# Kernel tuning notes

Hardware: AMD Instinct MI355X
Metric: run time of the kernel (lower is better)

The kernel has to match this reference:

```python
import jax, jax.numpy as jnp
import numpy as np


def _soft_attention(h, context, W_in, W_out):
    """Luong soft-dot attention. h: [B,H], context: [B,L,H].
    W_in: [H,H] (in,out layout), W_out: [2H,H]."""
    target = h @ W_in                                  # [B, H]
    attn = jnp.einsum('blh,bh->bl', context, target)   # [B, L]
    p = jax.nn.softmax(attn, axis=-1)                  # [B, L]
    weighted_ctx = jnp.einsum('bl,blh->bh', p, context)  # [B, H]
    h_tilde = jnp.tanh(jnp.concatenate([weighted_ctx, h], axis=1) @ W_out)  # [B, H]
    return h_tilde, p


def setup_inputs() -> dict:
    key = jax.random.key(0)
    ks = jax.random.split(key, 13)
    B, L, H = 64, 512, 1024
    s2 = 1.0 / np.sqrt(2 * H)
    s1 = 1.0 / np.sqrt(H)
    return {
        'h_tilde_s': jax.random.normal(ks[0], (B, H), jnp.float32),
        'h_tilde_o': jax.random.normal(ks[1], (B, H), jnp.float32),
        'h_tilde_a': jax.random.normal(ks[2], (B, H), jnp.float32),
        'enc_out': jax.random.normal(ks[3], (B, L, H), jnp.float32),
        'full_feature_len': 36,
        'W_as': jax.random.normal(ks[4], (2 * H, H), jnp.float32) * s2,
        'W_so': jax.random.normal(ks[5], (2 * H, H), jnp.float32) * s2,
        'W_oa': jax.random.normal(ks[6], (2 * H, H), jnp.float32) * s2,
        'Win_as': jax.random.normal(ks[7], (H, H), jnp.float32) * s1,
        'Win_so': jax.random.normal(ks[8], (H, H), jnp.float32) * s1,
        'Win_oa': jax.random.normal(ks[9], (H, H), jnp.float32) * s1,
        'Wout_as': jax.random.normal(ks[10], (2 * H, H), jnp.float32) * s2,
        'Wout_so': jax.random.normal(ks[11], (2 * H, H), jnp.float32) * s2,
        'Wout_oa': jax.random.normal(ks[12], (2 * H, H), jnp.float32) * s2,
    }


def reference(h_tilde_s, h_tilde_o, h_tilde_a, enc_out, full_feature_len,
              W_as, W_so, W_oa, Win_as, Win_so, Win_oa,
              Wout_as, Wout_so, Wout_oa):
    # Relational contexts via concat + linear(no bias) + tanh
    h_as = jnp.tanh(jnp.concatenate([h_tilde_a, h_tilde_s], axis=1) @ W_as)  # [B,H]
    h_so = jnp.tanh(jnp.concatenate([h_tilde_s, h_tilde_o], axis=1) @ W_so)
    h_oa = jnp.tanh(jnp.concatenate([h_tilde_o, h_tilde_a], axis=1) @ W_oa)
    # Three parallel soft-dot attentions over encoder output
    sa_as, _ = _soft_attention(h_as, enc_out, Win_as, Wout_as)
    sa_so, _ = _soft_attention(h_so, enc_out, Win_so, Wout_so)
    sa_oa, _ = _soft_attention(h_oa, enc_out, Win_oa, Wout_oa)
    B, H = sa_as.shape
    F = full_feature_len
    # repeat_interleave of size-1 dim == broadcast tile to [B, F, H]
    ctx_mas = jnp.broadcast_to(sa_as[:, None, :], (B, F, H))
    ctx_mso = jnp.broadcast_to(sa_so[:, None, :], (B, F, H))
    ctx_moa = jnp.broadcast_to(sa_oa[:, None, :], (B, F, H))
    return (ctx_mas, ctx_mso, ctx_moa)
```

## Files before the change

### kernel.cpp

```cpp
#include <hip/hip_runtime.h>

constexpr int BB = 64;
constexpr int LL = 512;
constexpr int HH = 1024;
constexpr int SPLITS = 16;
constexpr int NTHR  = 256;
constexpr int NWORK_GEMM = 3 * 16 * SPLITS;

typedef float nt_float4 __attribute__((ext_vector_type(4)));

struct Args {
    const float* hs; const float* ho; const float* ha; const float* enc;
    const int* Fp;
    const float* W_as;  const float* W_so;  const float* W_oa;
    const float* Win_as; const float* Win_so; const float* Win_oa;
    const float* Wout_as; const float* Wout_so; const float* Wout_oa;
    float* partA; float* partC; float* partG;
    float* hx; float* wc; float* opm; float* ms;
    float* out;
};

template<int K0, int K1>
__device__ __forceinline__ void gemm_tile(const float* __restrict__ a0,
                                          const float* __restrict__ a1,
                                          const float* __restrict__ w,
                                          float* __restrict__ part_r,
                                          int nt, int sp, int tid,
                                          float (*As)[64], float (*Ws)[64])
{
    constexpr int K = K0 + K1;
    constexpr int KRANGE = K / SPLITS;
    const int n0 = nt << 6;
    const int ks = sp * KRANGE;
    const int tn = tid & 15;
    const int tm = tid >> 4;
    const int m   = tid >> 2;
    const int kk0 = (tid & 3) << 3;
    const int j4  = (tid & 15) << 2;
    const int kkw = tid >> 4;

    float4 av0, av1, wv0, wv1;
    {
        const int kg = ks + kk0;
        const float* srcA = (K1 == 0 || kg < K0) ? (a0 + (size_t)m * HH + kg)
                                                 : (a1 + (size_t)m * HH + (kg - K0));
        av0 = *(const float4*)srcA;
        av1 = *(const float4*)(srcA + 4);
        wv0 = *(const float4*)(w + (size_t)(ks + kkw) * HH + n0 + j4);
        wv1 = *(const float4*)(w + (size_t)(ks + kkw + 16) * HH + n0 + j4);
    }

    float acc[4][4] = {};

    for (int kt = ks; kt < ks + KRANGE; kt += 32) {
        As[kk0 + 0][m] = av0.x; As[kk0 + 1][m] = av0.y;
        As[kk0 + 2][m] = av0.z; As[kk0 + 3][m] = av0.w;
        As[kk0 + 4][m] = av1.x; As[kk0 + 5][m] = av1.y;
        As[kk0 + 6][m] = av1.z; As[kk0 + 7][m] = av1.w;
        *(float4*)&Ws[kkw][j4]      = wv0;
        *(float4*)&Ws[kkw + 16][j4] = wv1;
        __syncthreads();

        if (kt + 32 < ks + KRANGE) {
            const int kn = kt + 32;
            const int kg = kn + kk0;
            const float* srcA = (K1 == 0 || kg < K0) ? (a0 + (size_t)m * HH + kg)
                                                     : (a1 + (size_t)m * HH + (kg - K0));
            av0 = *(const float4*)srcA;
            av1 = *(const float4*)(srcA + 4);
            wv0 = *(const float4*)(w + (size_t)(kn + kkw) * HH + n0 + j4);
            wv1 = *(const float4*)(w + (size_t)(kn + kkw + 16) * HH + n0 + j4);
        }

        #pragma unroll
        for (int kk = 0; kk < 32; kk++) {
            float4 a4 = *(const float4*)&As[kk][tm << 2];
            float4 b4 = *(const float4*)&Ws[kk][tn << 2];
            float av[4] = {a4.x, a4.y, a4.z, a4.w};
            float bv[4] = {b4.x, b4.y, b4.z, b4.w};
            #pragma unroll
            for (int i = 0; i < 4; i++)
                #pragma unroll
                for (int j = 0; j < 4; j++)
                    acc[i][j] += av[i] * bv[j];
        }
        __syncthreads();
    }

    float* dst = part_r + (size_t)(sp << 6) * HH + n0 + (tn << 2);
    #pragma unroll
    for (int i = 0; i < 4; i++) {
        const int mm = (tm << 2) + i;
        *(float4*)(dst + (size_t)mm * HH) = make_float4(acc[i][0], acc[i][1], acc[i][2], acc[i][3]);
    }
}

__global__ __launch_bounds__(NTHR)
void k_gemmA(Args a)
{
    __shared__ __align__(16) float smem[4096];
    const int wk = blockIdx.x, tid = threadIdx.x;
    const int r = wk >> 8, nt = wk & 15, sp = (wk >> 4) & 15;
    const float* a0 = (r == 0) ? a.ha : (r == 1) ? a.hs : a.ho;
    const float* a1 = (r == 0) ? a.hs : (r == 1) ? a.ho : a.ha;
    const float* w  = (r == 0) ? a.W_as : (r == 1) ? a.W_so : a.W_oa;
    gemm_tile<1024, 1024>(a0, a1, w, a.partA + (size_t)r * SPLITS * 65536,
                          nt, sp, tid, (float(*)[64])smem, (float(*)[64])(smem + 2048));
}

__global__ __launch_bounds__(NTHR)
void k_gemmC_fused(Args a)
{
    __shared__ __align__(16) float As2[64][64];
    __shared__ __align__(16) float Ws[32][64];
    const int wk = blockIdx.x, tid = threadIdx.x;
    const int r = wk >> 8, nt = wk & 15, sp = (wk >> 4) & 15;
    const int ks = sp << 6;
    const int n0 = nt << 6;
    const float* pA = a.partA + (size_t)r * SPLITS * 65536;
    const float* w  = (r == 0) ? a.Win_as : (r == 1) ? a.Win_so : a.Win_oa;

    #pragma unroll
    for (int i = 0; i < 4; i++) {
        const int s  = i * 256 + tid;
        const int m  = s >> 4;
        const int k4 = (s & 15) << 2;
        const float* p = pA + (size_t)m * HH + ks + k4;
        float4 v = *(const float4*)p;
        #pragma unroll 4
        for (int y = 1; y < SPLITS; y++) {
            float4 q = *(const float4*)(p + (size_t)y * 65536);
            v.x += q.x; v.y += q.y; v.z += q.z; v.w += q.w;
        }
        v.x = tanhf(v.x); v.y = tanhf(v.y); v.z = tanhf(v.z); v.w = tanhf(v.w);
        As2[k4 + 0][m] = v.x; As2[k4 + 1][m] = v.y;
        As2[k4 + 2][m] = v.z; As2[k4 + 3][m] = v.w;
        if (nt == 0)
            *(float4*)(a.hx + (size_t)r * 65536 + (size_t)m * HH + ks + k4) = v;
    }
    __syncthreads();

    const int tn = tid & 15, tm = tid >> 4;
    const int j4 = (tid & 15) << 2;
    const int kkw = tid >> 4;
    float acc[4][4] = {};
    float4 wv0 = *(const float4*)(w + (size_t)(ks + kkw) * HH + n0 + j4);
    float4 wv1 = *(const float4*)(w + (size_t)(ks + kkw + 16) * HH + n0 + j4);
    #pragma unroll
    for (int kt = 0; kt < 64; kt += 32) {
        *(float4*)&Ws[kkw][j4]      = wv0;
        *(float4*)&Ws[kkw + 16][j4] = wv1;
        __syncthreads();
        if (kt + 32 < 64) {
            wv0 = *(const float4*)(w + (size_t)(ks + kt + 32 + kkw) * HH + n0 + j4);
            wv1 = *(const float4*)(w + (size_t)(ks + kt + 32 + kkw + 16) * HH + n0 + j4);
        }
        #pragma unroll
        for (int kk = 0; kk < 32; kk++) {
            float4 a4 = *(const float4*)&As2[kt + kk][tm << 2];
            float4 b4 = *(const float4*)&Ws[kk][tn << 2];
            float av[4] = {a4.x, a4.y, a4.z, a4.w};
            float bv[4] = {b4.x, b4.y, b4.z, b4.w};
            #pragma unroll
            for (int i = 0; i < 4; i++)
                #pragma unroll
                for (int j = 0; j < 4; j++)
                    acc[i][j] += av[i] * bv[j];
        }
        __syncthreads();
    }

    float* dst = a.partC + (size_t)r * SPLITS * 65536
               + (size_t)(sp << 6) * HH + n0 + (tn << 2);
    #pragma unroll
    for (int i = 0; i < 4; i++) {
        const int mm = (tm << 2) + i;
        *(float4*)(dst + (size_t)mm * HH) = make_float4(acc[i][0], acc[i][1], acc[i][2], acc[i][3]);
    }
}

__global__ __launch_bounds__(NTHR)
void k_flash_fused(Args a)
{
    __shared__ __align__(16) float smem[3072 + 4096 + 32];
    float* tr_l = smem;
    float (*o_l)[HH]     = (float(*)[HH])(smem + 3072);
    float (*ms_sh)[3][2] = (float(*)[3][2])(smem + 3072 + 4096);
    const int chunk = blockIdx.x, tid = threadIdx.x;
    const int b    = chunk >> 3;
    const int lc   = chunk & 7;
    const int lane = tid & 63;
    const int wv   = tid >> 6;

    #pragma unroll
    for (int i = 0; i < 3; i++) {
        const int s  = i * 256 + tid;
        const int rr = s >> 8;
        const int h4 = (s & 255) << 2;
        const float* p = a.partC + (size_t)rr * SPLITS * 65536 + (size_t)b * HH + h4;
        float4 v = *(const float4*)p;
        #pragma unroll 4
        for (int y = 1; y < SPLITS; y++) {
            float4 q = *(const float4*)(p + (size_t)y * 65536);
            v.x += q.x; v.y += q.y; v.z += q.z; v.w += q.w;
        }
        *(float4*)&tr_l[rr * 1024 + h4] = v;
    }
    __syncthreads();

    float4 tr[3][4];
    #pragma unroll
    for (int r = 0; r < 3; r++)
        #pragma unroll
        for (int v = 0; v < 4; v++)
            tr[r][v] = *(const float4*)&tr_l[r * 1024 + (lane << 2) + (v << 8)];

    float  m_run[3] = {-3.0e38f, -3.0e38f, -3.0e38f};
    float  S_run[3] = {0.f, 0.f, 0.f};
    float4 o_run[3][4];
    #pragma unroll
    for (int r = 0; r < 3; r++)
        #pragma unroll
        for (int v = 0; v < 4; v++)
            o_run[r][v] = make_float4(0.f, 0.f, 0.f, 0.f);

    const float* ebase = a.enc + ((size_t)b * LL + (lc << 6) + (wv << 2)) * HH + (lane << 2);

    for (int it = 0; it < 4; it++) {
        const float* e = ebase + (size_t)(it << 4) * HH;
        float4 ev[4][4];
        #pragma unroll
        for (int j = 0; j < 4; j++)
            #pragma unroll
            for (int v = 0; v < 4; v++)
                ev[j][v] = *(const float4*)(e + (size_t)j * HH + (v << 8));

        float s[3][4];
        #pragma unroll
        for (int j = 0; j < 4; j++) {
            float d0 = 0.f, d1 = 0.f, d2 = 0.f;
            #pragma unroll
            for (int v = 0; v < 4; v++) {
                const float4 x = ev[j][v];
                d0 += x.x * tr[0][v].x + x.y * tr[0][v].y + x.z * tr[0][v].z + x.w * tr[0][v].w;
                d1 += x.x * tr[1][v].x + x.y * tr[1][v].y + x.z * tr[1][v].z + x.w * tr[1][v].w;
                d2 += x.x * tr[2][v].x + x.y * tr[2][v].y + x.z * tr[2][v].z + x.w * tr[2][v].w;
            }
            #pragma unroll
            for (int off = 32; off > 0; off >>= 1) {
                d0 += __shfl_xor(d0, off);
                d1 += __shfl_xor(d1, off);
                d2 += __shfl_xor(d2, off);
            }
            s[0][j] = d0; s[1][j] = d1; s[2][j] = d2;
        }

        #pragma unroll
        for (int r = 0; r < 3; r++) {
            const float mb = fmaxf(fmaxf(s[r][0], s[r][1]), fmaxf(s[r][2], s[r][3]));
            const float mn_ = fmaxf(m_run[r], mb);
            const float alpha = __expf(m_run[r] - mn_);
            m_run[r] = mn_;
            float p[4];
            float psum = 0.f;
            #pragma unroll
            for (int j = 0; j < 4; j++) { p[j] = __expf(s[r][j] - mn_); psum += p[j]; }
            S_run[r] = S_run[r] * alpha + psum;
            #pragma unroll
            for (int v = 0; v < 4; v++) {
                float4 o = o_run[r][v];
                o.x *= alpha; o.y *= alpha; o.z *= alpha; o.w *= alpha;
                #pragma unroll
                for (int j = 0; j < 4; j++) {
                    const float4 x = ev[j][v];
                    o.x += p[j] * x.x; o.y += p[j] * x.y;
                    o.z += p[j] * x.z; o.w += p[j] * x.w;
                }
                o_run[r][v] = o;
            }
        }
    }

    __syncthreads();
    if (lane == 0) {
        #pragma unroll
        for (int r = 0; r < 3; r++) { ms_sh[wv][r][0] = m_run[r]; ms_sh[wv][r][1] = S_run[r]; }
    }

    #pragma unroll
    for (int r = 0; r < 3; r++) {
        __syncthreads();
        #pragma unroll
        for (int v = 0; v < 4; v++)
            *(float4*)&o_l[wv][(lane << 2) + (v << 8)] = o_run[r][v];
        __syncthreads();

        const float m0 = ms_sh[0][r][0], m1 = ms_sh[1][r][0];
        const float m2 = ms_sh[2][r][0], m3 = ms_sh[3][r][0];
        const float M = fmaxf(fmaxf(m0, m1), fmaxf(m2, m3));
        const float w0 = __expf(m0 - M), w1 = __expf(m1 - M);
        const float w2 = __expf(m2 - M), w3 = __expf(m3 - M);
        float4 q0 = *(const float4*)&o_l[0][tid << 2];
        float4 q1 = *(const float4*)&o_l[1][tid << 2];
        float4 q2 = *(const float4*)&o_l[2][tid << 2];
        float4 q3 = *(const float4*)&o_l[3][tid << 2];
        float4 acc;
        acc.x = w0 * q0.x + w1 * q1.x + w2 * q2.x + w3 * q3.x;
        acc.y = w0 * q0.y + w1 * q1.y + w2 * q2.y + w3 * q3.y;
        acc.z = w0 * q0.z + w1 * q1.z + w2 * q2.z + w3 * q3.z;
        acc.w = w0 * q0.w + w1 * q1.w + w2 * q2.w + w3 * q3.w;
        *(float4*)&a.opm[((size_t)chunk * 3 + r) * HH + (tid << 2)] = acc;
        if (tid == 0) {
            const float S = w0 * ms_sh[0][r][1] + w1 * ms_sh[1][r][1]
                          + w2 * ms_sh[2][r][1] + w3 * ms_sh[3][r][1];
            a.ms[((size_t)chunk * 3 + r) * 2 + 0] = M;
            a.ms[((size_t)chunk * 3 + r) * 2 + 1] = S;
        }
    }
}

__global__ __launch_bounds__(NTHR)
void k_combine(Args a)
{
    const int b = blockIdx.x, r = blockIdx.y, tid = threadIdx.x;
    float mv[8], sv[8];
    float M = -3.0e38f;
    #pragma unroll
    for (int c = 0; c < 8; c++) {
        const int chunk = (b << 3) + c;
        mv[c] = a.ms[((size_t)chunk * 3 + r) * 2 + 0];
        sv[c] = a.ms[((size_t)chunk * 3 + r) * 2 + 1];
        M = fmaxf(M, mv[c]);
    }
    float S = 0.f;
    float4 acc = make_float4(0.f, 0.f, 0.f, 0.f);
    #pragma unroll
    for (int c = 0; c < 8; c++) {
        const float wgt = __expf(mv[c] - M);
        S += wgt * sv[c];
        const int chunk = (b << 3) + c;
        float4 q = *(const float4*)&a.opm[((size_t)chunk * 3 + r) * HH + (tid << 2)];
        acc.x += wgt * q.x; acc.y += wgt * q.y;
        acc.z += wgt * q.z; acc.w += wgt * q.w;
    }
    const float inv = 1.0f / S;
    acc.x *= inv; acc.y *= inv; acc.z *= inv; acc.w *= inv;
    *(float4*)&a.wc[(size_t)(r * BB + b) * HH + (tid << 2)] = acc;
}

__global__ __launch_bounds__(NTHR)
void k_gemmG(Args a)
{
    __shared__ __align__(16) float smem[4096];
    const int wk = blockIdx.x, tid = threadIdx.x;
    const int r = wk >> 8, nt = wk & 15, sp = (wk >> 4) & 15;
    const float* a0 = a.wc + (size_t)r * 65536;
    const float* a1 = a.hx + (size_t)r * 65536;
    const float* w  = (r == 0) ? a.Wout_as : (r == 1) ? a.Wout_so : a.Wout_oa;
    gemm_tile<1024, 1024>(a0, a1, w, a.partG + (size_t)r * SPLITS * 65536,
                          nt, sp, tid, (float(*)[64])smem, (float(*)[64])(smem + 2048));
}

__global__ __launch_bounds__(NTHR)
void k_bcast(Args a)
{
    const int i4   = blockIdx.x * NTHR + threadIdx.x;
    const int flat = i4 << 2;
    const int r    = flat >> 16;
    const int mn   = flat & 65535;
    const float* p = a.partG + (size_t)r * SPLITS * 65536 + mn;
    float4 s = *(const float4*)p;
    #pragma unroll
    for (int y = 1; y < SPLITS; y++) {
        float4 q = *(const float4*)(p + (size_t)y * 65536);
        s.x += q.x; s.y += q.y; s.z += q.z; s.w += q.w;
    }
    s.x = tanhf(s.x); s.y = tanhf(s.y); s.z = tanhf(s.z); s.w = tanhf(s.w);

    nt_float4 sv;
    sv.x = s.x; sv.y = s.y; sv.z = s.z; sv.w = s.w;

    const int F  = *a.Fp;
    const int bb = mn >> 10;
    const int hh = mn & 1023;
    float* o = a.out + ((size_t)(r * BB + bb) * F) * HH + hh;
    for (int f = 0; f < F; f++)
        __builtin_nontemporal_store(sv, (nt_float4*)(o + (size_t)f * HH));
}

extern "C" void kernel_launch(void* const* d_in, const int* in_sizes, int n_in,
                              void* d_out, int out_size, void* d_ws, size_t ws_size,
                              hipStream_t stream)
{
    (void)in_sizes; (void)n_in; (void)out_size; (void)ws_size;
    float* ws = (float*)d_ws;

    Args a;
    a.hs  = (const float*)d_in[0];
    a.ho  = (const float*)d_in[1];
    a.ha  = (const float*)d_in[2];
    a.enc = (const float*)d_in[3];
    a.Fp  = (const int*)d_in[4];
    a.W_as    = (const float*)d_in[5];
    a.W_so    = (const float*)d_in[6];
    a.W_oa    = (const float*)d_in[7];
    a.Win_as  = (const float*)d_in[8];
    a.Win_so  = (const float*)d_in[9];
    a.Win_oa  = (const float*)d_in[10];
    a.Wout_as = (const float*)d_in[11];
    a.Wout_so = (const float*)d_in[12];
    a.Wout_oa = (const float*)d_in[13];

    a.partA = ws;
    a.partC = ws + 3145728;
    a.partG = ws + 6291456;
    a.hx    = ws + 9437184;
    a.wc    = ws + 9633792;
    a.opm   = ws + 9830400;
    a.ms    = ws + 11403264;
    a.out   = (float*)d_out;

    k_gemmA      <<<NWORK_GEMM, NTHR, 0, stream>>>(a);
    k_gemmC_fused<<<NWORK_GEMM, NTHR, 0, stream>>>(a);
    k_flash_fused<<<512,        NTHR, 0, stream>>>(a);
    k_combine    <<<dim3(64, 3), NTHR, 0, stream>>>(a);
    k_gemmG      <<<NWORK_GEMM, NTHR, 0, stream>>>(a);
    k_bcast      <<<192,        NTHR, 0, stream>>>(a);
}
```

Baseline: 326.1 us.

## Raise parallelism: 512-thread GEMM tiles, finer flash chunks, split broadcast writes

The GEMM kernels move from 256 to 512 threads per block, with each thread computing a 2x4 micro-tile instead of 4x4 and loading a single float4 of each operand. The attention pass splits each batch row into 16 chunks of 32 positions instead of 8 chunks of 64, launching 1024 blocks, and the combine step merges 16 partials. The broadcast kernel splits the F-dimension stores across four blocks per element group. The aim is more waves in flight to hide memory latency on the wide GPU, at the cost of less register reuse per thread and more partial results to merge.

```diff
diff --git a/kernel.cpp b/kernel.cpp
--- a/kernel.cpp
+++ b/kernel.cpp
@@ -4,8 +4,8 @@
 constexpr int LL = 512;
 constexpr int HH = 1024;
 constexpr int SPLITS = 16;
-constexpr int NTHR  = 256;
 constexpr int NWORK_GEMM = 3 * 16 * SPLITS;
+constexpr int CHUNKS = 1024;
 
 typedef float nt_float4 __attribute__((ext_vector_type(4)));
 
@@ -21,81 +21,70 @@
 };
 
 template<int K0, int K1>
-__device__ __forceinline__ void gemm_tile(const float* __restrict__ a0,
-                                          const float* __restrict__ a1,
-                                          const float* __restrict__ w,
-                                          float* __restrict__ part_r,
-                                          int nt, int sp, int tid,
-                                          float (*As)[64], float (*Ws)[64])
+__device__ __forceinline__ void gemm_tile512(const float* __restrict__ a0,
+                                             const float* __restrict__ a1,
+                                             const float* __restrict__ w,
+                                             float* __restrict__ part_r,
+                                             int nt, int sp, int tid,
+                                             float (*As)[64], float (*Ws)[64])
 {
     constexpr int K = K0 + K1;
     constexpr int KRANGE = K / SPLITS;
     const int n0 = nt << 6;
     const int ks = sp * KRANGE;
-    const int tn = tid & 15;
-    const int tm = tid >> 4;
-    const int m   = tid >> 2;
-    const int kk0 = (tid & 3) << 3;
-    const int j4  = (tid & 15) << 2;
-    const int kkw = tid >> 4;
-
-    float4 av0, av1, wv0, wv1;
+    const int ma  = tid >> 3;
+    const int ka  = (tid & 7) << 2;
+    const int kw  = tid >> 4;
+    const int jw  = (tid & 15) << 2;
+    const int tn  = tid & 15;
+    const int m0  = (tid >> 4) << 1;
+
+    float4 av, wv;
     {
-        const int kg = ks + kk0;
-        const float* srcA = (K1 == 0 || kg < K0) ? (a0 + (size_t)m * HH + kg)
-                                                 : (a1 + (size_t)m * HH + (kg - K0));
-        av0 = *(const float4*)srcA;
-        av1 = *(const float4*)(srcA + 4);
-        wv0 = *(const float4*)(w + (size_t)(ks + kkw) * HH + n0 + j4);
-        wv1 = *(const float4*)(w + (size_t)(ks + kkw + 16) * HH + n0 + j4);
-    }
-
-    float acc[4][4] = {};
+        const int kg = ks + ka;
+        const float* srcA = (K1 == 0 || kg < K0) ? (a0 + (size_t)ma * HH + kg)
+                                                 : (a1 + (size_t)ma * HH + (kg - K0));
+        av = *(const float4*)srcA;
+        wv = *(const float4*)(w + (size_t)(ks + kw) * HH + n0 + jw);
+    }
+
+    float acc[2][4] = {};
 
     for (int kt = ks; kt < ks + KRANGE; kt += 32) {
-        As[kk0 + 0][m] = av0.x; As[kk0 + 1][m] = av0.y;
-        As[kk0 + 2][m] = av0.z; As[kk0 + 3][m] = av0.w;
-        As[kk0 + 4][m] = av1.x; As[kk0 + 5][m] = av1.y;
-        As[kk0 + 6][m] = av1.z; As[kk0 + 7][m] = av1.w;
-        *(float4*)&Ws[kkw][j4]      = wv0;
-        *(float4*)&Ws[kkw + 16][j4] = wv1;
+        As[ka + 0][ma] = av.x; As[ka + 1][ma] = av.y;
+        As[ka + 2][ma] = av.z; As[ka + 3][ma] = av.w;
+        *(float4*)&Ws[kw][jw] = wv;
         __syncthreads();
 
         if (kt + 32 < ks + KRANGE) {
             const int kn = kt + 32;
-            const int kg = kn + kk0;
-            const float* srcA = (K1 == 0 || kg < K0) ? (a0 + (size_t)m * HH + kg)
-                                                     : (a1 + (size_t)m * HH + (kg - K0));
-            av0 = *(const float4*)srcA;
-            av1 = *(const float4*)(srcA + 4);
-            wv0 = *(const float4*)(w + (size_t)(kn + kkw) * HH + n0 + j4);
-            wv1 = *(const float4*)(w + (size_t)(kn + kkw + 16) * HH + n0 + j4);
+            const int kg = kn + ka;
+            const float* srcA = (K1 == 0 || kg < K0) ? (a0 + (size_t)ma * HH + kg)
+                                                     : (a1 + (size_t)ma * HH + (kg - K0));
+            av = *(const float4*)srcA;
+            wv = *(const float4*)(w + (size_t)(kn + kw) * HH + n0 + jw);
         }
 
         #pragma unroll
         for (int kk = 0; kk < 32; kk++) {
-            float4 a4 = *(const float4*)&As[kk][tm << 2];
+            float2 a2 = *(const float2*)&As[kk][m0];
             float4 b4 = *(const float4*)&Ws[kk][tn << 2];
-            float av[4] = {a4.x, a4.y, a4.z, a4.w};
-            float bv[4] = {b4.x, b4.y, b4.z, b4.w};
-            #pragma unroll
-            for (int i = 0; i < 4; i++)
-                #pragma unroll
-                for (int j = 0; j < 4; j++)
-                    acc[i][j] += av[i] * bv[j];
-        }
-        __syncthreads();
-    }
-
-    float* dst = part_r + (size_t)(sp << 6) * HH + n0 + (tn << 2);
-    #pragma unroll
-    for (int i = 0; i < 4; i++) {
-        const int mm = (tm << 2) + i;
-        *(float4*)(dst + (size_t)mm * HH) = make_float4(acc[i][0], acc[i][1], acc[i][2], acc[i][3]);
-    }
-}
-
-__global__ __launch_bounds__(NTHR)
+            acc[0][0] += a2.x * b4.x; acc[0][1] += a2.x * b4.y;
+            acc[0][2] += a2.x * b4.z; acc[0][3] += a2.x * b4.w;
+            acc[1][0] += a2.y * b4.x; acc[1][1] += a2.y * b4.y;
+            acc[1][2] += a2.y * b4.z; acc[1][3] += a2.y * b4.w;
+        }
+        __syncthreads();
+    }
+
+    #pragma unroll
+    for (int i = 0; i < 2; i++) {
+        float* dst = part_r + (size_t)((sp << 6) + m0 + i) * HH + n0 + (tn << 2);
+        *(float4*)dst = make_float4(acc[i][0], acc[i][1], acc[i][2], acc[i][3]);
+    }
+}
+
+__global__ __launch_bounds__(512, 6)
 void k_gemmA(Args a)
 {
     __shared__ __align__(16) float smem[4096];
@@ -104,11 +93,11 @@
     const float* a0 = (r == 0) ? a.ha : (r == 1) ? a.hs : a.ho;
     const float* a1 = (r == 0) ? a.hs : (r == 1) ? a.ho : a.ha;
     const float* w  = (r == 0) ? a.W_as : (r == 1) ? a.W_so : a.W_oa;
-    gemm_tile<1024, 1024>(a0, a1, w, a.partA + (size_t)r * SPLITS * 65536,
-                          nt, sp, tid, (float(*)[64])smem, (float(*)[64])(smem + 2048));
-}
-
-__global__ __launch_bounds__(NTHR)
+    gemm_tile512<1024, 1024>(a0, a1, w, a.partA + (size_t)r * SPLITS * 65536,
+                             nt, sp, tid, (float(*)[64])smem, (float(*)[64])(smem + 2048));
+}
+
+__global__ __launch_bounds__(512, 6)
 void k_gemmC_fused(Args a)
 {
     __shared__ __align__(16) float As2[64][64];
@@ -121,8 +110,8 @@
     const float* w  = (r == 0) ? a.Win_as : (r == 1) ? a.Win_so : a.Win_oa;
 
     #pragma unroll
-    for (int i = 0; i < 4; i++) {
-        const int s  = i * 256 + tid;
+    for (int i = 0; i < 2; i++) {
+        const int s  = i * 512 + tid;
         const int m  = s >> 4;
         const int k4 = (s & 15) << 2;
         const float* p = pA + (size_t)m * HH + ks + k4;
@@ -140,46 +129,39 @@
     }
     __syncthreads();
 
-    const int tn = tid & 15, tm = tid >> 4;
-    const int j4 = (tid & 15) << 2;
-    const int kkw = tid >> 4;
-    float acc[4][4] = {};
-    float4 wv0 = *(const float4*)(w + (size_t)(ks + kkw) * HH + n0 + j4);
-    float4 wv1 = *(const float4*)(w + (size_t)(ks + kkw + 16) * HH + n0 + j4);
+    const int kw = tid >> 4;
+    const int jw = (tid & 15) << 2;
+    const int tn = tid & 15;
+    const int m0 = (tid >> 4) << 1;
+    float acc[2][4] = {};
+    float4 wv = *(const float4*)(w + (size_t)(ks + kw) * HH + n0 + jw);
     #pragma unroll
     for (int kt = 0; kt < 64; kt += 32) {
-        *(float4*)&Ws[kkw][j4]      = wv0;
-        *(float4*)&Ws[kkw + 16][j4] = wv1;
-        __syncthreads();
-        if (kt + 32 < 64) {
-            wv0 = *(const float4*)(w + (size_t)(ks + kt + 32 + kkw) * HH + n0 + j4);
-            wv1 = *(const float4*)(w + (size_t)(ks + kt + 32 + kkw + 16) * HH + n0 + j4);
-        }
+        *(float4*)&Ws[kw][jw] = wv;
+        __syncthreads();
+        if (kt + 32 < 64)
+            wv = *(const float4*)(w + (size_t)(ks + kt + 32 + kw) * HH + n0 + jw);
         #pragma unroll
         for (int kk = 0; kk < 32; kk++) {
-            float4 a4 = *(const float4*)&As2[kt + kk][tm << 2];
+            float2 a2 = *(const float2*)&As2[kt + kk][m0];
             float4 b4 = *(const float4*)&Ws[kk][tn << 2];
-            float av[4] = {a4.x, a4.y, a4.z, a4.w};
-            float bv[4] = {b4.x, b4.y, b4.z, b4.w};
-            #pragma unroll
-            for (int i = 0; i < 4; i++)
-                #pragma unroll
-                for (int j = 0; j < 4; j++)
-                    acc[i][j] += av[i] * bv[j];
-        }
-        __syncthreads();
-    }
-
-    float* dst = a.partC + (size_t)r * SPLITS * 65536
-               + (size_t)(sp << 6) * HH + n0 + (tn << 2);
-    #pragma unroll
-    for (int i = 0; i < 4; i++) {
-        const int mm = (tm << 2) + i;
-        *(float4*)(dst + (size_t)mm * HH) = make_float4(acc[i][0], acc[i][1], acc[i][2], acc[i][3]);
-    }
-}
-
-__global__ __launch_bounds__(NTHR)
+            acc[0][0] += a2.x * b4.x; acc[0][1] += a2.x * b4.y;
+            acc[0][2] += a2.x * b4.z; acc[0][3] += a2.x * b4.w;
+            acc[1][0] += a2.y * b4.x; acc[1][1] += a2.y * b4.y;
+            acc[1][2] += a2.y * b4.z; acc[1][3] += a2.y * b4.w;
+        }
+        __syncthreads();
+    }
+
+    #pragma unroll
+    for (int i = 0; i < 2; i++) {
+        float* dst = a.partC + (size_t)r * SPLITS * 65536
+                   + (size_t)((sp << 6) + m0 + i) * HH + n0 + (tn << 2);
+        *(float4*)dst = make_float4(acc[i][0], acc[i][1], acc[i][2], acc[i][3]);
+    }
+}
+
+__global__ __launch_bounds__(256)
 void k_flash_fused(Args a)
 {
     __shared__ __align__(16) float smem[3072 + 4096 + 32];
@@ -187,8 +169,8 @@
     float (*o_l)[HH]     = (float(*)[HH])(smem + 3072);
     float (*ms_sh)[3][2] = (float(*)[3][2])(smem + 3072 + 4096);
     const int chunk = blockIdx.x, tid = threadIdx.x;
-    const int b    = chunk >> 3;
-    const int lc   = chunk & 7;
+    const int b    = chunk >> 4;
+    const int lc   = chunk & 15;
     const int lane = tid & 63;
     const int wv   = tid >> 6;
 
@@ -224,9 +206,9 @@
         for (int v = 0; v < 4; v++)
             o_run[r][v] = make_float4(0.f, 0.f, 0.f, 0.f);
 
-    const float* ebase = a.enc + ((size_t)b * LL + (lc << 6) + (wv << 2)) * HH + (lane << 2);
-
-    for (int it = 0; it < 4; it++) {
+    const float* ebase = a.enc + ((size_t)b * LL + (lc << 5) + (wv << 2)) * HH + (lane << 2);
+
+    for (int it = 0; it < 2; it++) {
         const float* e = ebase + (size_t)(it << 4) * HH;
         float4 ev[4][4];
         #pragma unroll
@@ -319,15 +301,15 @@
     }
 }
 
-__global__ __launch_bounds__(NTHR)
+__global__ __launch_bounds__(256)
 void k_combine(Args a)
 {
     const int b = blockIdx.x, r = blockIdx.y, tid = threadIdx.x;
-    float mv[8], sv[8];
+    float mv[16], sv[16];
     float M = -3.0e38f;
     #pragma unroll
-    for (int c = 0; c < 8; c++) {
-        const int chunk = (b << 3) + c;
+    for (int c = 0; c < 16; c++) {
+        const int chunk = (b << 4) + c;
         mv[c] = a.ms[((size_t)chunk * 3 + r) * 2 + 0];
         sv[c] = a.ms[((size_t)chunk * 3 + r) * 2 + 1];
         M = fmaxf(M, mv[c]);
@@ -335,10 +317,10 @@
     float S = 0.f;
     float4 acc = make_float4(0.f, 0.f, 0.f, 0.f);
     #pragma unroll
-    for (int c = 0; c < 8; c++) {
+    for (int c = 0; c < 16; c++) {
         const float wgt = __expf(mv[c] - M);
         S += wgt * sv[c];
-        const int chunk = (b << 3) + c;
+        const int chunk = (b << 4) + c;
         float4 q = *(const float4*)&a.opm[((size_t)chunk * 3 + r) * HH + (tid << 2)];
         acc.x += wgt * q.x; acc.y += wgt * q.y;
         acc.z += wgt * q.z; acc.w += wgt * q.w;
@@ -348,7 +330,7 @@
     *(float4*)&a.wc[(size_t)(r * BB + b) * HH + (tid << 2)] = acc;
 }
 
-__global__ __launch_bounds__(NTHR)
+__global__ __launch_bounds__(512, 6)
 void k_gemmG(Args a)
 {
     __shared__ __align__(16) float smem[4096];
@@ -357,14 +339,15 @@
     const float* a0 = a.wc + (size_t)r * 65536;
     const float* a1 = a.hx + (size_t)r * 65536;
     const float* w  = (r == 0) ? a.Wout_as : (r == 1) ? a.Wout_so : a.Wout_oa;
-    gemm_tile<1024, 1024>(a0, a1, w, a.partG + (size_t)r * SPLITS * 65536,
-                          nt, sp, tid, (float(*)[64])smem, (float(*)[64])(smem + 2048));
-}
-
-__global__ __launch_bounds__(NTHR)
+    gemm_tile512<1024, 1024>(a0, a1, w, a.partG + (size_t)r * SPLITS * 65536,
+                             nt, sp, tid, (float(*)[64])smem, (float(*)[64])(smem + 2048));
+}
+
+__global__ __launch_bounds__(256)
 void k_bcast(Args a)
 {
-    const int i4   = blockIdx.x * NTHR + threadIdx.x;
+    const int bid  = blockIdx.x;
+    const int i4   = (bid >> 2) * 256 + threadIdx.x;
     const int flat = i4 << 2;
     const int r    = flat >> 16;
     const int mn   = flat & 65535;
@@ -381,10 +364,14 @@
     sv.x = s.x; sv.y = s.y; sv.z = s.z; sv.w = s.w;
 
     const int F  = *a.Fp;
+    const int fc = bid & 3;
+    const int fchunk = (F + 3) >> 2;
+    const int fb = fc * fchunk;
+    const int fe = (fb + fchunk < F) ? fb + fchunk : F;
     const int bb = mn >> 10;
     const int hh = mn & 1023;
     float* o = a.out + ((size_t)(r * BB + bb) * F) * HH + hh;
-    for (int f = 0; f < F; f++)
+    for (int f = fb; f < fe; f++)
         __builtin_nontemporal_store(sv, (nt_float4*)(o + (size_t)f * HH));
 }
 
@@ -417,13 +404,13 @@
     a.hx    = ws + 9437184;
     a.wc    = ws + 9633792;
     a.opm   = ws + 9830400;
-    a.ms    = ws + 11403264;
+    a.ms    = ws + 12976128;
     a.out   = (float*)d_out;
 
-    k_gemmA      <<<NWORK_GEMM, NTHR, 0, stream>>>(a);
-    k_gemmC_fused<<<NWORK_GEMM, NTHR, 0, stream>>>(a);
-    k_flash_fused<<<512,        NTHR, 0, stream>>>(a);
-    k_combine    <<<dim3(64, 3), NTHR, 0, stream>>>(a);
-    k_gemmG      <<<NWORK_GEMM, NTHR, 0, stream>>>(a);
-    k_bcast      <<<192,        NTHR, 0, stream>>>(a);
-}
+    k_gemmA      <<<NWORK_GEMM, 512, 0, stream>>>(a);
+    k_gemmC_fused<<<NWORK_GEMM, 512, 0, stream>>>(a);
+    k_flash_fused<<<CHUNKS,     256, 0, stream>>>(a);
+    k_combine    <<<dim3(64, 3), 256, 0, stream>>>(a);
+    k_gemmG      <<<NWORK_GEMM, 512, 0, stream>>>(a);
+    k_bcast      <<<768,        256, 0, stream>>>(a);
+}
```

After: 345.9 us. +6.1%, slower.
